# Kernel optimization log

Measured on AMD Instinct MI355X. Metric: run time of the kernel, lower is better.

The kernel has to match this reference:

```python
import jax, jax.numpy as jnp
import numpy as np

L, C, H = 12, 1024, 16  # n_layer, n_embd, n_head
D = C // H
EPS = 1e-5

def gelu_new(x):
    # GPT-2 tanh-approximate GELU
    return 0.5 * x * (1.0 + jnp.tanh(np.sqrt(2.0 / np.pi).astype(np.float32) * (x + 0.044715 * x ** 3)))

def layernorm(x, g, b):
    mu = jnp.mean(x, axis=-1, keepdims=True)
    var = jnp.mean(jnp.square(x - mu), axis=-1, keepdims=True)
    return (x - mu) * jax.lax.rsqrt(var + EPS) * g + b

def setup_inputs() -> dict:
    key = jax.random.key(0)
    ks = jax.random.split(key, 8)
    std = 0.02
    inp = {
        'inputs_embeds': jax.random.normal(ks[0], (1, 1024, C), jnp.float32),
        'attention_mask': jnp.ones((1, 1024), jnp.float32),
        'ln1_g': jnp.ones((L, C), jnp.float32), 'ln1_b': jnp.zeros((L, C), jnp.float32),
        'Wqkv': jax.random.normal(ks[1], (L, C, 3 * C), jnp.float32) * std,
        'bqkv': jnp.zeros((L, 3 * C), jnp.float32),
        'Wo': jax.random.normal(ks[2], (L, C, C), jnp.float32) * (std / np.sqrt(2 * L)),
        'bo': jnp.zeros((L, C), jnp.float32),
        'ln2_g': jnp.ones((L, C), jnp.float32), 'ln2_b': jnp.zeros((L, C), jnp.float32),
        'Wfc': jax.random.normal(ks[3], (L, C, 4 * C), jnp.float32) * std,
        'bfc': jnp.zeros((L, 4 * C), jnp.float32),
        'Wmp': jax.random.normal(ks[4], (L, 4 * C, C), jnp.float32) * (std / np.sqrt(2 * L)),
        'bmp': jnp.zeros((L, C), jnp.float32),
        'lnf_g': jnp.ones((C,), jnp.float32), 'lnf_b': jnp.zeros((C,), jnp.float32),
    }
    return inp

def reference(inputs_embeds, attention_mask, ln1_g, ln1_b, Wqkv, bqkv, Wo, bo,
              ln2_g, ln2_b, Wfc, bfc, Wmp, bmp, lnf_g, lnf_b):
    B, T, _ = inputs_embeds.shape
    # padding mask -> additive bias [B,1,1,T] (broadcasts over heads and query dim)
    mask_add = -1e9 * (1.0 - attention_mask)[:, None, None, :]
    scale = 1.0 / np.sqrt(D).astype(np.float32)

    def block(x, p):
        g1, b1, Wq, bq, Wo_, bo_, g2, b2, Wf, bf, Wm, bm = p
        h = layernorm(x, g1, b1)
        qkv = h @ Wq + bq                                  # [B,T,3C]
        q, k, v = jnp.split(qkv, 3, axis=-1)
        q = q.reshape(B, T, H, D).transpose(0, 2, 1, 3)    # [B,H,T,D]
        k = k.reshape(B, T, H, D).transpose(0, 2, 1, 3)
        v = v.reshape(B, T, H, D).transpose(0, 2, 1, 3)
        att = jnp.einsum('bhqd,bhkd->bhqk', q, k) * scale + mask_add
        att = jax.nn.softmax(att, axis=-1)
        y = jnp.einsum('bhqk,bhkd->bhqd', att, v)
        y = y.transpose(0, 2, 1, 3).reshape(B, T, C)
        x = x + (y @ Wo_ + bo_)
        h2 = layernorm(x, g2, b2)
        x = x + (gelu_new(h2 @ Wf + bf) @ Wm + bm)
        return x, None

    params = (ln1_g, ln1_b, Wqkv, bqkv, Wo, bo, ln2_g, ln2_b, Wfc, bfc, Wmp, bmp)
    x, _ = jax.lax.scan(block, inputs_embeds, params)
    return layernorm(x, lnf_g, lnf_b)
```

## Files before the change

kernel.cpp:

```cpp
#include <hip/hip_runtime.h>
#include <hip/hip_bf16.h>
#include <math.h>

#define LN_EPS 1e-5f

typedef unsigned short u16;
typedef __attribute__((ext_vector_type(8))) _Float16 f16x8;
typedef __attribute__((ext_vector_type(4))) float f32x4;

__device__ __forceinline__ u16 f2h(float x) {
    _Float16 h = (_Float16)x;
    return __builtin_bit_cast(u16, h);
}
__device__ __forceinline__ void stv(float* p, float v) { *p = v; }
__device__ __forceinline__ void stv(u16* p, float v) { *p = f2h(v); }
__device__ __forceinline__ void stv4(float* p, float a, float b, float c, float d) {
    *(float4*)p = make_float4(a, b, c, d);
}
__device__ __forceinline__ void stv4(u16* p, float a, float b, float c, float d) {
    ushort4 o; o.x = f2h(a); o.y = f2h(b); o.z = f2h(c); o.w = f2h(d);
    *(ushort4*)p = o;
}

__device__ __forceinline__ float gelu_f(float x) {
    const float kA = 0.7978845608028654f;
    return 0.5f * x * (1.f + tanhf(kA * (x + 0.044715f * x * x * x)));
}

__device__ __forceinline__ void gl_lds16(const u16* g, u16* l) {
    __builtin_amdgcn_global_load_lds(
        (const __attribute__((address_space(1))) unsigned int*)g,
        (__attribute__((address_space(3))) unsigned int*)l, 16, 0, 0);
}
template <int N> __device__ __forceinline__ void s_vmcnt() {
    asm volatile("s_waitcnt vmcnt(%0)" :: "n"(N) : "memory");
}
__device__ __forceinline__ void s_lgkm0() {
    asm volatile("s_waitcnt lgkmcnt(0)" ::: "memory");
    __builtin_amdgcn_sched_barrier(0);
}
__device__ __forceinline__ void bar() { __builtin_amdgcn_s_barrier(); }
__device__ __forceinline__ void sfence() { __builtin_amdgcn_sched_barrier(0); }

template <int PART, typename OT>
__global__ __launch_bounds__(256) void ln_kernel(float* __restrict__ x,
                                                 const float* __restrict__ p0,
                                                 const float* __restrict__ p1,
                                                 const float* __restrict__ gam,
                                                 const float* __restrict__ bet,
                                                 OT* __restrict__ out) {
    int w = threadIdx.x >> 6, lane = threadIdx.x & 63;
    int row = blockIdx.x * 4 + w;
    size_t base = (size_t)row * 1024;
    float4 v[4];
    float s = 0.f, ss = 0.f;
#pragma unroll
    for (int j = 0; j < 4; j++) {
        int c = lane * 4 + j * 256;
        float4 xv = *(const float4*)(x + base + c);
        if (PART) {
            float4 a = *(const float4*)(p0 + base + c);
            float4 b = *(const float4*)(p1 + base + c);
            xv.x += a.x + b.x; xv.y += a.y + b.y;
            xv.z += a.z + b.z; xv.w += a.w + b.w;
            *(float4*)(x + base + c) = xv;
        }
        v[j] = xv;
        s += xv.x + xv.y + xv.z + xv.w;
        ss += xv.x * xv.x + xv.y * xv.y + xv.z * xv.z + xv.w * xv.w;
    }
#pragma unroll
    for (int off = 32; off > 0; off >>= 1) {
        s += __shfl_xor(s, off);
        ss += __shfl_xor(ss, off);
    }
    float mu = s * (1.f / 1024.f);
    float var = ss * (1.f / 1024.f) - mu * mu;
    float rstd = rsqrtf(var + LN_EPS);
#pragma unroll
    for (int j = 0; j < 4; j++) {
        int c = lane * 4 + j * 256;
        float4 gv = *(const float4*)(gam + c);
        float4 bv = *(const float4*)(bet + c);
        stv4(&out[base + c],
             (v[j].x - mu) * rstd * gv.x + bv.x,
             (v[j].y - mu) * rstd * gv.y + bv.y,
             (v[j].z - mu) * rstd * gv.z + bv.z,
             (v[j].w - mu) * rstd * gv.w + bv.w);
    }
}

__global__ __launch_bounds__(256) void tr_cvt_all(
    const float* __restrict__ Wqkv, const float* __restrict__ Wo,
    const float* __restrict__ Wfc, const float* __restrict__ Wmp,
    u16* __restrict__ wq, u16* __restrict__ wo,
    u16* __restrict__ wf, u16* __restrict__ wm) {
    int id = blockIdx.x;
    const float* W; u16* Wt; int K, N, idx;
    if (id < 768)       { W = Wqkv; Wt = wq; K = 1024; N = 3072; idx = id; }
    else if (id < 1024) { W = Wo;   Wt = wo; K = 1024; N = 1024; idx = id - 768; }
    else if (id < 2048) { W = Wfc;  Wt = wf; K = 1024; N = 4096; idx = id - 1024; }
    else                { W = Wmp;  Wt = wm; K = 4096; N = 1024; idx = id - 2048; }
    int ntn = N >> 6;
    int n0 = (idx % ntn) * 64, k0 = (idx / ntn) * 64;

    __shared__ float tile[64][65];
    int t = threadIdx.x;
    int r = t >> 4, c4 = (t & 15) * 4;
#pragma unroll
    for (int p = 0; p < 4; p++) {
        float4 v = *(const float4*)(W + (size_t)(k0 + p * 16 + r) * N + n0 + c4);
        tile[p * 16 + r][c4 + 0] = v.x;
        tile[p * 16 + r][c4 + 1] = v.y;
        tile[p * 16 + r][c4 + 2] = v.z;
        tile[p * 16 + r][c4 + 3] = v.w;
    }
    __syncthreads();
#pragma unroll
    for (int p = 0; p < 4; p++) {
        int n = p * 16 + r;
        ushort4 o;
        o.x = f2h(tile[c4 + 0][n]);
        o.y = f2h(tile[c4 + 1][n]);
        o.z = f2h(tile[c4 + 2][n]);
        o.w = f2h(tile[c4 + 3][n]);
        *(ushort4*)(Wt + (size_t)(n0 + n) * K + k0 + c4) = o;
    }
}

template <int BM, int BN, int BK, int WROW, int WCOL, int ACT, int WVT, int SPLITK,
          typename OT>
__global__ __launch_bounds__(WROW * WCOL * 64) void gemm_f16(
    const u16* __restrict__ A, const u16* __restrict__ Bt,
    const float* __restrict__ bias, OT* __restrict__ out,
    u16* __restrict__ vTout, int M, int N, int K) {
    __shared__ u16 As[2][BM * BK];
    __shared__ u16 Bs[2][BN * BK];
    constexpr int THREADS = WROW * WCOL * 64;
    constexpr int WM = BM / WROW, WN = BN / WCOL;
    constexpr int FM = WM / 16, FN = WN / 16;
    constexpr int NKF = BK / 32;
    constexpr int SLOTS = BK / 8;
    constexpr int ACH = BM * BK / 8 / THREADS;
    constexpr int BCH = BN * BK / 8 / THREADS;
    constexpr int LPS = ACH + BCH;
    int tid = threadIdx.x;
    int w = tid >> 6, l = tid & 63;
    int wm = w / WCOL, wn = w % WCOL;
    int lr = l & 15, g = l >> 4;
    int m0 = blockIdx.y * BM, n0 = blockIdx.x * BN;
    int kbase = (SPLITK > 1) ? blockIdx.z * (K / SPLITK) : 0;
    int Kc = (SPLITK > 1) ? (K / SPLITK) : K;
    OT* outz = (SPLITK > 1) ? out + (size_t)blockIdx.z * M * N : out;

    f32x4 acc[FM][FN] = {};

    auto stage = [&](int buf, int k0) {
#pragma unroll
        for (int i = 0; i < ACH; i++) {
            int chunk = i * THREADS + tid;
            int row = chunk / SLOTS, s = chunk % SLOTS, sg = s ^ (row & 7);
            gl_lds16(A + (size_t)(m0 + row) * K + kbase + k0 + sg * 8, &As[buf][chunk * 8]);
        }
#pragma unroll
        for (int i = 0; i < BCH; i++) {
            int chunk = i * THREADS + tid;
            int row = chunk / SLOTS, s = chunk % SLOTS, sg = s ^ (row & 7);
            gl_lds16(Bt + (size_t)(n0 + row) * K + kbase + k0 + sg * 8, &Bs[buf][chunk * 8]);
        }
    };

    int NT = Kc / BK;
    stage(0, 0);
    int cur = 0;
    for (int t = 0; t < NT; t++) {
        if (t + 1 < NT) { stage(cur ^ 1, (t + 1) * BK); s_vmcnt<LPS>(); }
        else            { s_vmcnt<0>(); }
        bar();
        sfence();

        const u16* Ab = &As[cur][0];
        const u16* Bb = &Bs[cur][0];
        f16x8 af[FM][NKF], bfrag[FN][NKF];
#pragma unroll
        for (int m = 0; m < FM; m++)
#pragma unroll
            for (int kf = 0; kf < NKF; kf++) {
                int row = wm * WM + m * 16 + lr;
                af[m][kf] = *(const f16x8*)(Ab + row * BK + (((kf * 4 + g) ^ (row & 7)) * 8));
            }
#pragma unroll
        for (int n = 0; n < FN; n++)
#pragma unroll
            for (int kf = 0; kf < NKF; kf++) {
                int row = wn * WN + n * 16 + lr;
                bfrag[n][kf] = *(const f16x8*)(Bb + row * BK + (((kf * 4 + g) ^ (row & 7)) * 8));
            }
#pragma unroll
        for (int kf = 0; kf < NKF; kf++)
#pragma unroll
            for (int m = 0; m < FM; m++)
#pragma unroll
                for (int n = 0; n < FN; n++)
                    acc[m][n] = __builtin_amdgcn_mfma_f32_16x16x32_f16(
                        af[m][kf], bfrag[n][kf], acc[m][n], 0, 0, 0);

        sfence();
        bar();
        cur ^= 1;
    }

#pragma unroll
    for (int m = 0; m < FM; m++) {
#pragma unroll
        for (int n = 0; n < FN; n++) {
            int col = n0 + wn * WN + n * 16 + lr;
            int row0 = m0 + wm * WM + m * 16 + 4 * g;
            float bv = (SPLITK > 1 && blockIdx.z != 0) ? 0.f : bias[col];
            u16 hv[4];
#pragma unroll
            for (int r = 0; r < 4; r++) {
                float v = acc[m][n][r] + bv;
                if (ACT) v = gelu_f(v);
                stv(&outz[(size_t)(row0 + r) * N + col], v);
                if (WVT) hv[r] = f2h(v);
            }
            if (WVT && col >= 2048) {
                ushort4 pv; pv.x = hv[0]; pv.y = hv[1]; pv.z = hv[2]; pv.w = hv[3];
                *(ushort4*)(vTout + (size_t)(col - 2048) * 1024 + row0) = pv;
            }
        }
    }
}

__global__ __launch_bounds__(256) void attn_mfma(
    const u16* __restrict__ qkv, const u16* __restrict__ vT,
    const float* __restrict__ mask, u16* __restrict__ y) {
    int h = blockIdx.y;
    int q0 = blockIdx.x * 64;
    int tid = threadIdx.x;
    int w = tid >> 6, l = tid & 63;
    int lr = l & 15, g = l >> 4;

    __shared__ u16 Ks[2][128 * 64];
    __shared__ u16 Vs[2][64 * 128];
    __shared__ u16 Ps[4 * 16 * 128];
    __shared__ float maskb[1024];

    for (int i = tid; i < 1024; i += 256) maskb[i] = -1e9f * (1.f - mask[i]);
    s_lgkm0();

    f16x8 qf[2];
#pragma unroll
    for (int kf = 0; kf < 2; kf++)
        qf[kf] = *(const f16x8*)(qkv + (size_t)(q0 + w * 16 + lr) * 3072 + h * 64 + kf * 32 + g * 8);

    f32x4 o[4] = {};
    float mrow[4], lrow[4];
#pragma unroll
    for (int r = 0; r < 4; r++) { mrow[r] = -1e30f; lrow[r] = 0.f; }

    u16* Psw = Ps + w * 2048;

    auto stage = [&](int buf, int kc) {
#pragma unroll
        for (int i = 0; i < 4; i++) {
            int chunk = i * 256 + tid;
            int krow = chunk >> 3, ks = chunk & 7, ksg = ks ^ (krow & 7);
            gl_lds16(qkv + (size_t)(kc * 128 + krow) * 3072 + 1024 + h * 64 + ksg * 8,
                     &Ks[buf][chunk * 8]);
            int vrow = chunk >> 4, vs = chunk & 15, vsg = vs ^ (vrow & 7);
            gl_lds16(vT + (size_t)(h * 64 + vrow) * 1024 + kc * 128 + vsg * 8,
                     &Vs[buf][chunk * 8]);
        }
    };

    stage(0, 0);
    int cur = 0;
    for (int kc = 0; kc < 8; kc++) {
        if (kc + 1 < 8) { stage(cur ^ 1, kc + 1); s_vmcnt<8>(); }
        else            { s_vmcnt<0>(); }
        bar();
        sfence();
        const u16* Kb = &Ks[cur][0];
        const u16* Vb = &Vs[cur][0];

        f32x4 s[8] = {};
        __builtin_amdgcn_s_setprio(1);
#pragma unroll
        for (int n = 0; n < 8; n++)
#pragma unroll
            for (int kf = 0; kf < 2; kf++) {
                int row = n * 16 + lr;
                f16x8 kfrag = *(const f16x8*)(Kb + row * 64 + (((kf * 4 + g) ^ (row & 7)) * 8));
                s[n] = __builtin_amdgcn_mfma_f32_16x16x32_f16(qf[kf], kfrag, s[n], 0, 0, 0);
            }
        __builtin_amdgcn_s_setprio(0);

        float mcol[8];
#pragma unroll
        for (int n = 0; n < 8; n++) mcol[n] = maskb[kc * 128 + n * 16 + lr];

        float scl[4], mnew[4], psum[4];
#pragma unroll
        for (int r = 0; r < 4; r++) {
            float mx = -1e30f;
#pragma unroll
            for (int n = 0; n < 8; n++) {
                float sv = s[n][r] * 0.125f + mcol[n];
                s[n][r] = sv;
                mx = fmaxf(mx, sv);
            }
            mx = fmaxf(mx, __shfl_xor(mx, 1));
            mx = fmaxf(mx, __shfl_xor(mx, 2));
            mx = fmaxf(mx, __shfl_xor(mx, 4));
            mx = fmaxf(mx, __shfl_xor(mx, 8));
            mnew[r] = fmaxf(mrow[r], mx);
            scl[r] = __expf(mrow[r] - mnew[r]);
            mrow[r] = mnew[r];
            psum[r] = 0.f;
        }
#pragma unroll
        for (int n = 0; n < 8; n++) {
            float p0 = __expf(s[n][0] - mnew[0]);
            float p1 = __expf(s[n][1] - mnew[1]);
            float p2 = __expf(s[n][2] - mnew[2]);
            float p3 = __expf(s[n][3] - mnew[3]);
            psum[0] += p0; psum[1] += p1; psum[2] += p2; psum[3] += p3;
            int col = n * 16 + lr, cs = col >> 3, cl = col & 7;
            int r0 = 4 * g;
            Psw[(r0 + 0) * 128 + ((cs ^ ((r0 + 0) & 7)) * 8) + cl] = f2h(p0);
            Psw[(r0 + 1) * 128 + ((cs ^ ((r0 + 1) & 7)) * 8) + cl] = f2h(p1);
            Psw[(r0 + 2) * 128 + ((cs ^ ((r0 + 2) & 7)) * 8) + cl] = f2h(p2);
            Psw[(r0 + 3) * 128 + ((cs ^ ((r0 + 3) & 7)) * 8) + cl] = f2h(p3);
        }
#pragma unroll
        for (int r = 0; r < 4; r++) {
            float ps_ = psum[r];
            ps_ += __shfl_xor(ps_, 1);
            ps_ += __shfl_xor(ps_, 2);
            ps_ += __shfl_xor(ps_, 4);
            ps_ += __shfl_xor(ps_, 8);
            lrow[r] = lrow[r] * scl[r] + ps_;
#pragma unroll
            for (int dn = 0; dn < 4; dn++) o[dn][r] *= scl[r];
        }

        f16x8 pa[4];
#pragma unroll
        for (int kf = 0; kf < 4; kf++)
            pa[kf] = *(const f16x8*)(Psw + lr * 128 + (((kf * 4 + g) ^ (lr & 7)) * 8));
        __builtin_amdgcn_s_setprio(1);
#pragma unroll
        for (int dn = 0; dn < 4; dn++) {
#pragma unroll
            for (int kf = 0; kf < 4; kf++) {
                int row = dn * 16 + lr;
                f16x8 vb = *(const f16x8*)(Vb + row * 128 + (((kf * 4 + g) ^ (row & 7)) * 8));
                o[dn] = __builtin_amdgcn_mfma_f32_16x16x32_f16(pa[kf], vb, o[dn], 0, 0, 0);
            }
        }
        __builtin_amdgcn_s_setprio(0);

        sfence();
        bar();
        cur ^= 1;
    }

    float inv[4];
#pragma unroll
    for (int r = 0; r < 4; r++) inv[r] = 1.f / lrow[r];
#pragma unroll
    for (int dn = 0; dn < 4; dn++)
#pragma unroll
        for (int r = 0; r < 4; r++) {
            int row = q0 + w * 16 + 4 * g + r;
            int col = h * 64 + dn * 16 + lr;
            y[(size_t)row * 1024 + col] = f2h(o[dn][r] * inv[r]);
        }
}

extern "C" void kernel_launch(void* const* d_in, const int* in_sizes, int n_in,
                              void* d_out, int out_size, void* d_ws, size_t ws_size,
                              hipStream_t stream) {
    const float* inputs_embeds = (const float*)d_in[0];
    const float* attn_mask     = (const float*)d_in[1];
    const float* ln1_g = (const float*)d_in[2];
    const float* ln1_b = (const float*)d_in[3];
    const float* Wqkv  = (const float*)d_in[4];
    const float* bqkv  = (const float*)d_in[5];
    const float* Wo    = (const float*)d_in[6];
    const float* bo    = (const float*)d_in[7];
    const float* ln2_g = (const float*)d_in[8];
    const float* ln2_b = (const float*)d_in[9];
    const float* Wfc   = (const float*)d_in[10];
    const float* bfc   = (const float*)d_in[11];
    const float* Wmp   = (const float*)d_in[12];
    const float* bmp   = (const float*)d_in[13];
    const float* lnf_g = (const float*)d_in[14];
    const float* lnf_b = (const float*)d_in[15];
    float* out = (float*)d_out;

    char* ws = (char*)d_ws;
    float* x   = (float*)ws;
    u16* hbuf  = (u16*)(ws + (4u << 20));
    u16* qkvb  = (u16*)(ws + (6u << 20));
    u16* fcb   = qkvb;
    u16* ybuf  = hbuf;
    u16* vTb   = (u16*)(ws + (14u << 20));
    u16* wq    = (u16*)(ws + (16u << 20));
    u16* wo_   = (u16*)(ws + (22u << 20));
    u16* wf    = (u16*)(ws + (24u << 20));
    u16* wm    = (u16*)(ws + (32u << 20));
    float* pP  = (float*)(ws + (40u << 20));
    float* pM  = (float*)(ws + (48u << 20));

    hipMemcpyAsync(x, inputs_embeds, (size_t)(1 << 20) * sizeof(float),
                   hipMemcpyDeviceToDevice, stream);

    for (int l = 0; l < 12; l++) {
        tr_cvt_all<<<3072, 256, 0, stream>>>(
            Wqkv + (size_t)l * 3145728, Wo + (size_t)l * 1048576,
            Wfc + (size_t)l * 4194304, Wmp + (size_t)l * 4194304,
            wq, wo_, wf, wm);

        if (l == 0)
            ln_kernel<0, u16><<<256, 256, 0, stream>>>(
                x, nullptr, nullptr, ln1_g + l * 1024, ln1_b + l * 1024, hbuf);
        else
            ln_kernel<1, u16><<<256, 256, 0, stream>>>(
                x, pM, pM + (1 << 20), ln1_g + l * 1024, ln1_b + l * 1024, hbuf);

        gemm_f16<64, 128, 64, 2, 4, 0, 1, 1, u16><<<dim3(24, 16), 512, 0, stream>>>(
            hbuf, wq, bqkv + (size_t)l * 3072, qkvb, vTb, 1024, 3072, 1024);
        attn_mfma<<<dim3(16, 16), 256, 0, stream>>>(qkvb, vTb, attn_mask, ybuf);
        gemm_f16<64, 64, 128, 2, 2, 0, 0, 2, float><<<dim3(16, 16, 2), 256, 0, stream>>>(
            ybuf, wo_, bo + (size_t)l * 1024, pP, nullptr, 1024, 1024, 1024);
        ln_kernel<1, u16><<<256, 256, 0, stream>>>(
            x, pP, pP + (1 << 20), ln2_g + l * 1024, ln2_b + l * 1024, hbuf);
        gemm_f16<128, 128, 64, 2, 4, 1, 0, 1, u16><<<dim3(32, 8), 512, 0, stream>>>(
            hbuf, wf, bfc + (size_t)l * 4096, fcb, nullptr, 1024, 4096, 1024);
        gemm_f16<64, 64, 128, 2, 2, 0, 0, 2, float><<<dim3(16, 16, 2), 256, 0, stream>>>(
            fcb, wm, bmp + (size_t)l * 1024, pM, nullptr, 1024, 1024, 4096);
    }
    ln_kernel<1, float><<<256, 256, 0, stream>>>(x, pM, pM + (1 << 20), lnf_g, lnf_b, out);
}
```

Baseline: 1.359 ms.

## Double-buffer weight conversion and fold next layer's transpose into layernorm launches

Converting weights from fp32 to transposed fp16 for layer l+1 is now done by extra blocks appended to the two layernorm launches of layer l, writing into alternating double buffers. Only layer 0 still uses a standalone conversion kernel. This removes one kernel launch per layer and lets the bandwidth-bound conversion share a launch with the small layernorm grid, filling idle CUs. The cost is a larger workspace for the two weight buffers, and the layernorm launches become heavier, which could slow the layernorm rows that sit on the critical path.

```diff
diff --git a/kernel.cpp b/kernel.cpp
--- a/kernel.cpp
+++ b/kernel.cpp
@@ -42,13 +42,66 @@
 __device__ __forceinline__ void bar() { __builtin_amdgcn_s_barrier(); }
 __device__ __forceinline__ void sfence() { __builtin_amdgcn_sched_barrier(0); }
 
+__device__ __forceinline__ void cvt_tile(int t, const float* __restrict__ Wqkv,
+                                         const float* __restrict__ Wo,
+                                         const float* __restrict__ Wfc,
+                                         const float* __restrict__ Wmp,
+                                         u16* __restrict__ dst, float (*tile)[65]) {
+    const float* W; u16* Wt; int K, N, idx;
+    if (t < 768)       { W = Wqkv; Wt = dst;           K = 1024; N = 3072; idx = t; }
+    else if (t < 1024) { W = Wo;   Wt = dst + 3145728; K = 1024; N = 1024; idx = t - 768; }
+    else if (t < 2048) { W = Wfc;  Wt = dst + 4194304; K = 1024; N = 4096; idx = t - 1024; }
+    else               { W = Wmp;  Wt = dst + 8388608; K = 4096; N = 1024; idx = t - 2048; }
+    int ntn = N >> 6;
+    int n0 = (idx % ntn) * 64, k0 = (idx / ntn) * 64;
+    int th = threadIdx.x;
+    int r = th >> 4, c4 = (th & 15) * 4;
+#pragma unroll
+    for (int p = 0; p < 4; p++) {
+        float4 v = *(const float4*)(W + (size_t)(k0 + p * 16 + r) * N + n0 + c4);
+        tile[p * 16 + r][c4 + 0] = v.x;
+        tile[p * 16 + r][c4 + 1] = v.y;
+        tile[p * 16 + r][c4 + 2] = v.z;
+        tile[p * 16 + r][c4 + 3] = v.w;
+    }
+    __syncthreads();
+#pragma unroll
+    for (int p = 0; p < 4; p++) {
+        int n = p * 16 + r;
+        ushort4 o;
+        o.x = f2h(tile[c4 + 0][n]);
+        o.y = f2h(tile[c4 + 1][n]);
+        o.z = f2h(tile[c4 + 2][n]);
+        o.w = f2h(tile[c4 + 3][n]);
+        *(ushort4*)(Wt + (size_t)(n0 + n) * K + k0 + c4) = o;
+    }
+}
+
+__global__ __launch_bounds__(256) void tr_cvt_all(
+    const float* __restrict__ Wqkv, const float* __restrict__ Wo,
+    const float* __restrict__ Wfc, const float* __restrict__ Wmp,
+    u16* __restrict__ dst) {
+    __shared__ float tile[64][65];
+    cvt_tile(blockIdx.x, Wqkv, Wo, Wfc, Wmp, dst, tile);
+}
+
 template <int PART, typename OT>
-__global__ __launch_bounds__(256) void ln_kernel(float* __restrict__ x,
-                                                 const float* __restrict__ p0,
-                                                 const float* __restrict__ p1,
-                                                 const float* __restrict__ gam,
-                                                 const float* __restrict__ bet,
-                                                 OT* __restrict__ out) {
+__global__ __launch_bounds__(256) void ln_cvt(float* __restrict__ x,
+                                              const float* __restrict__ p0,
+                                              const float* __restrict__ p1,
+                                              const float* __restrict__ gam,
+                                              const float* __restrict__ bet,
+                                              OT* __restrict__ out,
+                                              const float* __restrict__ cWq,
+                                              const float* __restrict__ cWo,
+                                              const float* __restrict__ cWf,
+                                              const float* __restrict__ cWm,
+                                              u16* __restrict__ cdst, int cbase) {
+    __shared__ float tile[64][65];
+    if (blockIdx.x >= 256) {
+        cvt_tile(blockIdx.x - 256 + cbase, cWq, cWo, cWf, cWm, cdst, tile);
+        return;
+    }
     int w = threadIdx.x >> 6, lane = threadIdx.x & 63;
     int row = blockIdx.x * 4 + w;
     size_t base = (size_t)row * 1024;
@@ -87,44 +140,6 @@
              (v[j].y - mu) * rstd * gv.y + bv.y,
              (v[j].z - mu) * rstd * gv.z + bv.z,
              (v[j].w - mu) * rstd * gv.w + bv.w);
-    }
-}
-
-__global__ __launch_bounds__(256) void tr_cvt_all(
-    const float* __restrict__ Wqkv, const float* __restrict__ Wo,
-    const float* __restrict__ Wfc, const float* __restrict__ Wmp,
-    u16* __restrict__ wq, u16* __restrict__ wo,
-    u16* __restrict__ wf, u16* __restrict__ wm) {
-    int id = blockIdx.x;
-    const float* W; u16* Wt; int K, N, idx;
-    if (id < 768)       { W = Wqkv; Wt = wq; K = 1024; N = 3072; idx = id; }
-    else if (id < 1024) { W = Wo;   Wt = wo; K = 1024; N = 1024; idx = id - 768; }
-    else if (id < 2048) { W = Wfc;  Wt = wf; K = 1024; N = 4096; idx = id - 1024; }
-    else                { W = Wmp;  Wt = wm; K = 4096; N = 1024; idx = id - 2048; }
-    int ntn = N >> 6;
-    int n0 = (idx % ntn) * 64, k0 = (idx / ntn) * 64;
-
-    __shared__ float tile[64][65];
-    int t = threadIdx.x;
-    int r = t >> 4, c4 = (t & 15) * 4;
-#pragma unroll
-    for (int p = 0; p < 4; p++) {
-        float4 v = *(const float4*)(W + (size_t)(k0 + p * 16 + r) * N + n0 + c4);
-        tile[p * 16 + r][c4 + 0] = v.x;
-        tile[p * 16 + r][c4 + 1] = v.y;
-        tile[p * 16 + r][c4 + 2] = v.z;
-        tile[p * 16 + r][c4 + 3] = v.w;
-    }
-    __syncthreads();
-#pragma unroll
-    for (int p = 0; p < 4; p++) {
-        int n = p * 16 + r;
-        ushort4 o;
-        o.x = f2h(tile[c4 + 0][n]);
-        o.y = f2h(tile[c4 + 1][n]);
-        o.z = f2h(tile[c4 + 2][n]);
-        o.w = f2h(tile[c4 + 3][n]);
-        *(ushort4*)(Wt + (size_t)(n0 + n) * K + k0 + c4) = o;
     }
 }
 
@@ -408,40 +423,51 @@
     u16* fcb   = qkvb;
     u16* ybuf  = hbuf;
     u16* vTb   = (u16*)(ws + (14u << 20));
-    u16* wq    = (u16*)(ws + (16u << 20));
-    u16* wo_   = (u16*)(ws + (22u << 20));
-    u16* wf    = (u16*)(ws + (24u << 20));
-    u16* wm    = (u16*)(ws + (32u << 20));
-    float* pP  = (float*)(ws + (40u << 20));
-    float* pM  = (float*)(ws + (48u << 20));
+    u16* wbuf0 = (u16*)(ws + (16u << 20));
+    u16* wbuf1 = (u16*)(ws + (40u << 20));
+    float* pP  = (float*)(ws + (64u << 20));
+    float* pM  = (float*)(ws + (72u << 20));
 
     hipMemcpyAsync(x, inputs_embeds, (size_t)(1 << 20) * sizeof(float),
                    hipMemcpyDeviceToDevice, stream);
 
+    tr_cvt_all<<<3072, 256, 0, stream>>>(Wqkv, Wo, Wfc, Wmp, wbuf0);
+
     for (int l = 0; l < 12; l++) {
-        tr_cvt_all<<<3072, 256, 0, stream>>>(
-            Wqkv + (size_t)l * 3145728, Wo + (size_t)l * 1048576,
-            Wfc + (size_t)l * 4194304, Wmp + (size_t)l * 4194304,
-            wq, wo_, wf, wm);
+        u16* wb = (l & 1) ? wbuf1 : wbuf0;
+        u16* wq = wb, *wo_ = wb + 3145728, *wf = wb + 4194304, *wm = wb + 8388608;
+
+        bool cv = (l + 1 < 12);
+        u16* nb = ((l + 1) & 1) ? wbuf1 : wbuf0;
+        const float* nWq = cv ? Wqkv + (size_t)(l + 1) * 3145728 : nullptr;
+        const float* nWo = cv ? Wo   + (size_t)(l + 1) * 1048576 : nullptr;
+        const float* nWf = cv ? Wfc  + (size_t)(l + 1) * 4194304 : nullptr;
+        const float* nWm = cv ? Wmp  + (size_t)(l + 1) * 4194304 : nullptr;
+        int grid_ln = cv ? 256 + 1536 : 256;
 
         if (l == 0)
-            ln_kernel<0, u16><<<256, 256, 0, stream>>>(
-                x, nullptr, nullptr, ln1_g + l * 1024, ln1_b + l * 1024, hbuf);
+            ln_cvt<0, u16><<<grid_ln, 256, 0, stream>>>(
+                x, nullptr, nullptr, ln1_g + l * 1024, ln1_b + l * 1024, hbuf,
+                nWq, nWo, nWf, nWm, nb, 0);
         else
-            ln_kernel<1, u16><<<256, 256, 0, stream>>>(
-                x, pM, pM + (1 << 20), ln1_g + l * 1024, ln1_b + l * 1024, hbuf);
+            ln_cvt<1, u16><<<grid_ln, 256, 0, stream>>>(
+                x, pM, pM + (1 << 20), ln1_g + l * 1024, ln1_b + l * 1024, hbuf,
+                nWq, nWo, nWf, nWm, nb, 0);
 
         gemm_f16<64, 128, 64, 2, 4, 0, 1, 1, u16><<<dim3(24, 16), 512, 0, stream>>>(
             hbuf, wq, bqkv + (size_t)l * 3072, qkvb, vTb, 1024, 3072, 1024);
         attn_mfma<<<dim3(16, 16), 256, 0, stream>>>(qkvb, vTb, attn_mask, ybuf);
         gemm_f16<64, 64, 128, 2, 2, 0, 0, 2, float><<<dim3(16, 16, 2), 256, 0, stream>>>(
             ybuf, wo_, bo + (size_t)l * 1024, pP, nullptr, 1024, 1024, 1024);
-        ln_kernel<1, u16><<<256, 256, 0, stream>>>(
-            x, pP, pP + (1 << 20), ln2_g + l * 1024, ln2_b + l * 1024, hbuf);
+        ln_cvt<1, u16><<<grid_ln, 256, 0, stream>>>(
+            x, pP, pP + (1 << 20), ln2_g + l * 1024, ln2_b + l * 1024, hbuf,
+            nWq, nWo, nWf, nWm, nb, 1536);
         gemm_f16<128, 128, 64, 2, 4, 1, 0, 1, u16><<<dim3(32, 8), 512, 0, stream>>>(
             hbuf, wf, bfc + (size_t)l * 4096, fcb, nullptr, 1024, 4096, 1024);
         gemm_f16<64, 64, 128, 2, 2, 0, 0, 2, float><<<dim3(16, 16, 2), 256, 0, stream>>>(
             fcb, wm, bmp + (size_t)l * 1024, pM, nullptr, 1024, 1024, 4096);
     }
-    ln_kernel<1, float><<<256, 256, 0, stream>>>(x, pM, pM + (1 << 20), lnf_g, lnf_b, out);
-}
+    ln_cvt<1, float><<<256, 256, 0, stream>>>(
+        x, pM, pM + (1 << 20), lnf_g, lnf_b, out,
+        nullptr, nullptr, nullptr, nullptr, nullptr, 0);
+}
```

Result: no change. 1.334 ms (median of 3 runs) (-1.9%).
